# Optimization experiments

Measured on AMD Instinct MI355X. Metric: run time of the kernel, lower is better.

Reference implementation:

```python
import jax, jax.numpy as jnp
import numpy as np

NUM_HEADS = 16


def setup_inputs() -> dict:
    key = jax.random.key(0)
    ks = jax.random.split(key, 7)
    dim, hd = 1024, 64
    B, H, W = 64, 14, 14  # B = batch * num_windows, 14x14 window
    x = jax.random.normal(ks[0], (B, H, W, dim), dtype=jnp.float32)
    qkv_w = jax.random.normal(ks[1], (dim, 3 * dim), dtype=jnp.float32) * (dim ** -0.5)
    qkv_b = jnp.zeros((3 * dim,), dtype=jnp.float32)
    proj_w = jax.random.normal(ks[2], (dim, dim), dtype=jnp.float32) * (dim ** -0.5)
    proj_b = jnp.zeros((dim,), dtype=jnp.float32)
    rel_pos_h = jax.random.normal(ks[3], (2 * H - 1, hd), dtype=jnp.float32) * 0.02
    rel_pos_w = jax.random.normal(ks[4], (2 * W - 1, hd), dtype=jnp.float32) * 0.02
    return {"x": x, "qkv_w": qkv_w, "qkv_b": qkv_b, "proj_w": proj_w,
            "proj_b": proj_b, "rel_pos_h": rel_pos_h, "rel_pos_w": rel_pos_w}


def reference(x, qkv_w, qkv_b, proj_w, proj_b, rel_pos_h, rel_pos_w):
    B, H, W, dim = x.shape
    nH = NUM_HEADS
    hd = dim // nH
    scale = hd ** -0.5

    # qkv projection: [B, HW, 3*dim]
    qkv = x.reshape(B, H * W, dim) @ qkv_w + qkv_b
    # -> [3, nH, B, HW, hd] -> [3, nH*B, HW, hd]
    qkv = qkv.reshape(B, H * W, 3, nH, hd).transpose(2, 3, 0, 1, 4)
    qkv = qkv.reshape(3, nH * B, H * W, hd)
    q, k, v = qkv[0], qkv[1], qkv[2]

    # scaled QK^T: [nH*B, HW, HW]
    attn = jnp.einsum('bqc,bkc->bqk', q * scale, k)

    # decomposed relative position bias (q_size == k_size, no interpolation)
    Rh = rel_pos_h[jnp.arange(H)[:, None] - jnp.arange(H)[None, :] + (H - 1)]  # [H,H,hd]
    Rw = rel_pos_w[jnp.arange(W)[:, None] - jnp.arange(W)[None, :] + (W - 1)]  # [W,W,hd]
    r_q = q.reshape(nH * B, H, W, hd)
    rel_h = jnp.einsum('bhwc,hkc->bhwk', r_q, Rh)  # [nH*B,H,W,H]
    rel_w = jnp.einsum('bhwc,wkc->bhwk', r_q, Rw)  # [nH*B,H,W,W]
    attn = (attn.reshape(nH * B, H, W, H, W)
            + rel_h[:, :, :, :, None]
            + rel_w[:, :, :, None, :]).reshape(nH * B, H * W, H * W)

    attn = jax.nn.softmax(attn, axis=-1)
    out = attn @ v  # [nH*B, HW, hd]

    # merge heads: [nH,B,H,W,hd] -> [B,H,W,dim]
    out = out.reshape(nH, B, H, W, hd).transpose(1, 2, 3, 0, 4).reshape(B, H, W, dim)
    return out @ proj_w + proj_b
```

## Files before the change

### kernel.cpp

```cpp
#include <hip/hip_runtime.h>
#include <cstdint>
#include <cstddef>

typedef unsigned short u16;
typedef unsigned int u32;
typedef float f32x4 __attribute__((ext_vector_type(4)));
typedef short short8 __attribute__((ext_vector_type(8)));
typedef u32 u32x2 __attribute__((ext_vector_type(2)));

#define HW 196
#define DIM 1024
#define HD 64
#define SP 208
#define SPV 224
#define NBH 1024

__device__ __forceinline__ float bf2f(u16 x){
  union { u32 u; float f; } c; c.u = ((u32)x) << 16; return c.f;
}
__device__ __forceinline__ u16 f2bf(float f){
  union { float f; u32 u; } c; c.f = f;
  return (u16)((c.u + 0x7fffu + ((c.u >> 16) & 1u)) >> 16);
}
__device__ __forceinline__ u32 cvtpk_bf16(float lo, float hi){
  u32 r;
  asm("v_cvt_pk_bf16_f32 %0, %1, %2" : "=v"(r) : "v"(lo), "v"(hi));
  return r;
}
#define LGKM_FENCE() do { \
    asm volatile("s_waitcnt lgkmcnt(0)" ::: "memory"); \
    __builtin_amdgcn_sched_barrier(0); \
  } while (0)
#define DS_FENCE() do { \
    asm volatile("s_waitcnt lgkmcnt(0)" ::: "memory"); \
    __builtin_amdgcn_sched_barrier(0x7F); \
  } while (0)
#define WAITV4() asm volatile("s_waitcnt vmcnt(4)" ::: "memory")
#define BAR() __builtin_amdgcn_s_barrier()

typedef __attribute__((address_space(3))) void lds_void_t;
typedef __attribute__((address_space(1))) const void glb_void_t;
__device__ __forceinline__ void gload_lds16(const void* g, void* l){
  __builtin_amdgcn_global_load_lds((glb_void_t*)g, (lds_void_t*)l, 16, 0, 0);
}

__global__ __launch_bounds__(256) void k_xcvt(const float* __restrict__ x,
                                              u16* __restrict__ xb, int n8){
  int i = blockIdx.x * 256 + threadIdx.x;
  if (i < n8){
    const f32x4* p = (const f32x4*)(x + (size_t)i * 8);
    f32x4 v0 = p[0], v1 = p[1];
    short8 t;
    #pragma unroll
    for (int e = 0; e < 4; ++e){
      t[e]   = (short)f2bf(v0[e]);
      t[4+e] = (short)f2bf(v1[e]);
    }
    *(short8*)(xb + (size_t)i * 8) = t;
  }
}

__global__ __launch_bounds__(256) void k_rprep(const float* __restrict__ rph,
                                               const float* __restrict__ rpw,
                                               u16* __restrict__ rphb,
                                               u16* __restrict__ rpwb){
  int r = threadIdx.x >> 3, cc = (threadIdx.x & 7) * 8;
  #pragma unroll
  for (int t = 0; t < 2; ++t){
    const float* src = t ? rpw : rph;
    u16* dst = t ? rpwb : rphb;
    short8 v;
    #pragma unroll
    for (int e = 0; e < 8; ++e)
      v[e] = (r < 27) ? (short)f2bf(src[(size_t)r * 64 + cc + e]) : (short)0;
    *(short8*)(dst + (size_t)r * 64 + cc) = v;
  }
}

__global__ __launch_bounds__(256) void k_wT(const float* __restrict__ w,
                                            u16* __restrict__ wT, int K, int N){
  __shared__ float t[32][33];
  int n0 = blockIdx.x * 32, k0 = blockIdx.y * 32;
  int c = threadIdx.x & 31, rr = threadIdx.x >> 5;
  #pragma unroll
  for (int i = 0; i < 4; ++i){
    int r = rr + i*8;
    t[r][c] = w[(size_t)(k0 + r) * N + n0 + c];
  }
  __syncthreads();
  #pragma unroll
  for (int i = 0; i < 4; ++i){
    int r = rr + i*8;
    wT[(size_t)(n0 + r) * K + k0 + c] = f2bf(t[c][r]);
  }
}

template<int MODE, bool SW>
__global__ __launch_bounds__(512, 2) void k_g256(const u16* __restrict__ Ab,
    const u16* __restrict__ Bt, const float* __restrict__ bias,
    u16* __restrict__ qg, u16* __restrict__ kg, u16* __restrict__ vTg,
    float* __restrict__ outf, int K, int N, int ntm, int ntn, int cyoff)
{
  extern __shared__ __align__(16) u16 smem[];
  const int tid = threadIdx.x;
  const int lane = tid & 63, wv = tid >> 6;
  const int wr = wv >> 2, wc = wv & 3;
  const int l16 = lane & 15, lk = lane >> 4;

  const int nwg = ntm * ntn;
  int bid = blockIdx.x;
  int q8 = nwg >> 3, r8 = nwg & 7;
  int xcd = bid & 7, loc = bid >> 3;
  int wgid = (xcd < r8 ? xcd*(q8+1) : r8*(q8+1) + (xcd - r8)*q8) + loc;
  int gsz = 8 * ntn;
  int g = wgid / gsz, rem = wgid - g * gsz;
  int gm = ntm - g * 8; if (gm > 8) gm = 8;
  int ry = g * 8 + rem % gm;
  int cy = rem / gm;
  const size_t m0 = (size_t)ry * 256;
  const size_t n0 = (size_t)(cyoff + cy) * 256;
  const int nk = K >> 6;

  auto off = [&](int d, int ab, int ks){ return ((d*2 + ab)*2 + ks) * 8192; };

  auto stageH = [&](int d, int ab, int ks, int tile){
    const u16* src = ab ? Bt : Ab;
    size_t rb = ab ? n0 : m0;
    int c = (lane & 3) ^ ((lane >> 3) & 3);
    #pragma unroll
    for (int i = 0; i < 2; ++i){
      int rh = 32*wv + 16*i + (lane >> 2);
      gload_lds16(src + (rb + rh) * (size_t)K + tile*64 + ks*32 + c*8,
                  smem + off(d, ab, ks) + (32*wv + 16*i) * 32);
    }
  };
  auto ldA = [&](short8* a, int d, int ks, int h){
    #pragma unroll
    for (int m2 = 0; m2 < 4; ++m2){
      int r = wr*128 + h*64 + m2*16 + l16;
      a[m2] = *(const short8*)(smem + off(d,0,ks) + r*32 + ((lk ^ ((r>>1)&3)) << 3));
    }
  };
  auto ldB = [&](short8* b, int d, int ks){
    #pragma unroll
    for (int ni = 0; ni < 4; ++ni){
      int r = wc*64 + ni*16 + l16;
      b[ni] = *(const short8*)(smem + off(d,1,ks) + r*32 + ((lk ^ ((r>>1)&3)) << 3));
    }
  };

  f32x4 acc[8][4] = {};
  auto mm = [&](int h, short8* a, short8* b){
    __builtin_amdgcn_s_setprio(1);
    #pragma unroll
    for (int m2 = 0; m2 < 4; ++m2)
      #pragma unroll
      for (int ni = 0; ni < 4; ++ni){
        if constexpr (SW)
          acc[h*4+m2][ni] = __builtin_amdgcn_mfma_f32_16x16x32_bf16(b[ni], a[m2], acc[h*4+m2][ni], 0, 0, 0);
        else
          acc[h*4+m2][ni] = __builtin_amdgcn_mfma_f32_16x16x32_bf16(a[m2], b[ni], acc[h*4+m2][ni], 0, 0, 0);
      }
    __builtin_amdgcn_s_setprio(0);
  };

  stageH(0, 0, 0, 0); stageH(0, 1, 0, 0); stageH(0, 0, 1, 0); stageH(0, 1, 1, 0);
  WAITV4(); BAR();

  #pragma unroll 1
  for (int kt = 0; kt < nk; ++kt){
    const int d = kt & 1, dn = d ^ 1;
    const int tn = (kt + 1 < nk) ? kt + 1 : nk - 1;
    short8 a[4], b0[4], b1[4];
    ldA(a, d, 0, 0); ldB(b0, d, 0);
    stageH(dn, 0, 0, tn);
    BAR(); LGKM_FENCE();
    mm(0, a, b0);
    BAR();
    ldA(a, d, 0, 1);
    stageH(dn, 1, 0, tn);
    WAITV4();
    BAR(); LGKM_FENCE();
    mm(1, a, b0);
    BAR();
    ldA(a, d, 1, 0); ldB(b1, d, 1);
    stageH(dn, 0, 1, tn);
    BAR(); LGKM_FENCE();
    mm(0, a, b1);
    BAR();
    ldA(a, d, 1, 1);
    stageH(dn, 1, 1, tn);
    WAITV4();
    BAR(); LGKM_FENCE();
    mm(1, a, b1);
    BAR();
  }

  const int rowb = (int)m0 + wr*128;
  const int colb = (int)n0 + wc*64;
  if constexpr (MODE == 1){
    #pragma unroll
    for (int mi = 0; mi < 8; ++mi){
      int r = rowb + mi*16 + l16;
      float* orow = outf + (size_t)r * N;
      #pragma unroll
      for (int ni = 0; ni < 4; ++ni){
        int c0 = colb + ni*16 + lk*4;
        f32x4 bz = *(const f32x4*)(bias + c0);
        f32x4 v = acc[mi][ni] + bz;
        *(f32x4*)(orow + c0) = v;
      }
    }
  } else if constexpr (SW){
    const int t3 = colb >> 10;
    u16* dst0 = (t3 == 0) ? qg : kg;
    const float sc = (t3 == 0) ? 1.0f : 0.125f;
    #pragma unroll
    for (int mi = 0; mi < 8; ++mi){
      int r = rowb + mi*16 + l16;
      int b = r / 196, n = r - b * 196;
      #pragma unroll
      for (int ni = 0; ni < 4; ++ni){
        int rr2 = ((colb & 1023) + ni*16);
        int hh = rr2 >> 6, ccb = (rr2 & 63) + lk*4;
        const float* bz = bias + colb + ni*16 + lk*4;
        u32 w0 = cvtpk_bf16((acc[mi][ni][0] + bz[0])*sc, (acc[mi][ni][1] + bz[1])*sc);
        u32 w1 = cvtpk_bf16((acc[mi][ni][2] + bz[2])*sc, (acc[mi][ni][3] + bz[3])*sc);
        u32* dst = (u32*)(dst0 + ((size_t)(hh*64 + b) * SP + n) * HD + ccb);
        dst[0] = w0; dst[1] = w1;
      }
    }
  } else {
    #pragma unroll
    for (int mi = 0; mi < 8; ++mi){
      int r4 = rowb + mi*16 + lk*4;
      int b = r4 / 196, n4 = r4 - b * 196;
      #pragma unroll
      for (int ni = 0; ni < 4; ++ni){
        int rr2 = ((colb & 1023) + ni*16);
        int hh = rr2 >> 6, cc = (rr2 & 63) + l16;
        float bz = bias[colb + ni*16 + l16];
        u32 w0 = cvtpk_bf16(acc[mi][ni][0] + bz, acc[mi][ni][1] + bz);
        u32 w1 = cvtpk_bf16(acc[mi][ni][2] + bz, acc[mi][ni][3] + bz);
        u32* dst = (u32*)(vTg + ((size_t)(hh*64 + b) * HD + cc) * SPV + n4);
        dst[0] = w0; dst[1] = w1;
      }
    }
  }
}

__global__ __launch_bounds__(256) void k_attn(
    const u16* __restrict__ qg, const u16* __restrict__ kg, const u16* __restrict__ vTg,
    const u16* __restrict__ rphb, const u16* __restrict__ rpwb,
    u16* __restrict__ ao)
{
  __shared__ __align__(16) char smem[4 * 7424];
  const int tid = threadIdx.x, lane = tid & 63, wvi = tid >> 6;
  const int l16 = lane & 15, lk = lane >> 4;
  char*  wbase = smem + wvi * 7424;
  float* relT  = (float*)wbase;
  u32*   Pp    = (u32*)wbase;

  int b = blockIdx.x;
  int sb = (b & 7) * 416 + (b >> 3);
  int j  = sb * 4 + wvi;
  int bh = j / 13;
  int mt = j - bh * 13;
  const int hh = bh >> 6, bb = bh & 63;
  const u16* qb = qg  + (size_t)bh * SP * HD;
  const u16* kb = kg  + (size_t)bh * SP * HD;
  const u16* vb = vTg + (size_t)bh * HD * SPV;

  const short8 a0 = *(const short8*)(qb + (size_t)(mt*16 + l16) * HD + lk*8);
  const short8 a1 = *(const short8*)(qb + (size_t)(mt*16 + l16) * HD + 32 + lk*8);

  {
    f32x4 z = {0.f,0.f,0.f,0.f};
    f32x4 racc[2][2] = {{z,z},{z,z}};
    #pragma unroll
    for (int dt = 0; dt < 2; ++dt){
      short8 h0 = *(const short8*)(rphb + (size_t)(dt*16 + l16) * 64 + lk*8);
      short8 h1 = *(const short8*)(rphb + (size_t)(dt*16 + l16) * 64 + 32 + lk*8);
      short8 w0 = *(const short8*)(rpwb + (size_t)(dt*16 + l16) * 64 + lk*8);
      short8 w1 = *(const short8*)(rpwb + (size_t)(dt*16 + l16) * 64 + 32 + lk*8);
      racc[0][dt] = __builtin_amdgcn_mfma_f32_16x16x32_bf16(h0, a0, racc[0][dt], 0, 0, 0);
      racc[0][dt] = __builtin_amdgcn_mfma_f32_16x16x32_bf16(h1, a1, racc[0][dt], 0, 0, 0);
      racc[1][dt] = __builtin_amdgcn_mfma_f32_16x16x32_bf16(w0, a0, racc[1][dt], 0, 0, 0);
      racc[1][dt] = __builtin_amdgcn_mfma_f32_16x16x32_bf16(w1, a1, racc[1][dt], 0, 0, 0);
    }
    #pragma unroll
    for (int t = 0; t < 2; ++t)
      #pragma unroll
      for (int dt = 0; dt < 2; ++dt)
        *(f32x4*)(relT + l16*68 + t*32 + dt*16 + lk*4) = racc[t][dt];
  }
  DS_FENCE();

  int qr = mt*16 + l16;
  int qrc = qr > HW-1 ? HW-1 : qr;
  int qh = qrc / 14, qw = qrc - 14*qh;
  const float* rrow = relT + l16*68;
  const int dh0 = qh + 13, dw0 = 32 + qw + 13;
  const int lk4 = lk*4;

  f32x4 sacc[13];
  #pragma unroll
  for (int nt = 0; nt < 13; ++nt){
    #pragma unroll
    for (int i = 0; i < 4; ++i){
      int k = nt*16 + lk4 + i;
      int kh = (k * 4682) >> 16;
      if (nt == 12 && kh > 13) kh = 13;
      int kw = k - kh*14;
      float bias = rrow[dh0 - kh] + rrow[dw0 - kw];
      sacc[nt][i] = (nt == 12 && lk != 0) ? -1e30f : bias;
    }
  }

  #pragma unroll
  for (int nt = 0; nt < 13; ++nt){
    int row = nt*16 + l16;
    short8 b0 = *(const short8*)(kb + (size_t)row * HD + lk*8);
    short8 b1 = *(const short8*)(kb + (size_t)row * HD + 32 + lk*8);
    sacc[nt] = __builtin_amdgcn_mfma_f32_16x16x32_bf16(b0, a0, sacc[nt], 0, 0, 0);
    sacc[nt] = __builtin_amdgcn_mfma_f32_16x16x32_bf16(b1, a1, sacc[nt], 0, 0, 0);
  }

  float m;
  {
    float t0[13];
    #pragma unroll
    for (int nt = 0; nt < 13; ++nt)
      t0[nt] = fmaxf(fmaxf(sacc[nt][0], sacc[nt][1]), fmaxf(sacc[nt][2], sacc[nt][3]));
    float a01 = fmaxf(t0[0], t0[1]),  a23 = fmaxf(t0[2], t0[3]);
    float a45 = fmaxf(t0[4], t0[5]),  a67 = fmaxf(t0[6], t0[7]);
    float a89 = fmaxf(t0[8], t0[9]),  aab = fmaxf(t0[10], t0[11]);
    m = fmaxf(fmaxf(fmaxf(a01, a23), fmaxf(a45, a67)), fmaxf(fmaxf(a89, aab), t0[12]));
  }
  m = fmaxf(m, __shfl_xor(m, 16, 64));
  m = fmaxf(m, __shfl_xor(m, 32, 64));
  float sum;
  {
    float s4[13];
    #pragma unroll
    for (int nt = 0; nt < 13; ++nt){
      #pragma unroll
      for (int i = 0; i < 4; ++i)
        sacc[nt][i] = __expf(sacc[nt][i] - m);
      s4[nt] = (sacc[nt][0] + sacc[nt][1]) + (sacc[nt][2] + sacc[nt][3]);
    }
    float b01 = s4[0]+s4[1], b23 = s4[2]+s4[3], b45 = s4[4]+s4[5];
    float b67 = s4[6]+s4[7], b89 = s4[8]+s4[9], bab = s4[10]+s4[11];
    sum = ((b01+b23) + (b45+b67)) + ((b89+bab) + s4[12]);
  }
  sum += __shfl_xor(sum, 16, 64);
  sum += __shfl_xor(sum, 32, 64);
  float inv = 1.0f / sum;

  DS_FENCE();
  u32* prow = Pp + l16*116;
  #pragma unroll
  for (int nt = 0; nt < 13; ++nt){
    u32x2 wpk;
    wpk[0] = cvtpk_bf16(sacc[nt][0], sacc[nt][1]);
    wpk[1] = cvtpk_bf16(sacc[nt][2], sacc[nt][3]);
    *(u32x2*)(prow + nt*8 + lk*2) = wpk;
  }
  { u32x2 zz = {0u, 0u}; *(u32x2*)(prow + 104 + lk*2) = zz; }
  DS_FENCE();

  f32x4 z = {0.f,0.f,0.f,0.f};
  f32x4 oacc[4] = {z,z,z,z};
  #pragma unroll
  for (int kt = 0; kt < 7; ++kt){
    short8 pa = *(const short8*)(prow + kt*16 + lk4);
    #pragma unroll
    for (int dt = 0; dt < 4; ++dt){
      short8 bv = *(const short8*)(vb + (size_t)(dt*16 + l16) * SPV + kt*32 + lk*8);
      oacc[dt] = __builtin_amdgcn_mfma_f32_16x16x32_bf16(bv, pa, oacc[dt], 0, 0, 0);
    }
  }
  int qrow = mt*16 + l16;
  if (qrow < HW){
    u16* orow = ao + ((size_t)bb * HW + qrow) * DIM + hh * HD;
    #pragma unroll
    for (int dt = 0; dt < 4; ++dt){
      u32 lo = cvtpk_bf16(oacc[dt][0]*inv, oacc[dt][1]*inv);
      u32 hi = cvtpk_bf16(oacc[dt][2]*inv, oacc[dt][3]*inv);
      u32* dst = (u32*)(orow + dt*16 + lk4);
      dst[0] = lo; dst[1] = hi;
    }
  }
}

extern "C" void kernel_launch(void* const* d_in, const int* in_sizes, int n_in,
                              void* d_out, int out_size, void* d_ws, size_t ws_size,
                              hipStream_t stream)
{
  const float* x      = (const float*)d_in[0];
  const float* qkv_w  = (const float*)d_in[1];
  const float* qkv_b  = (const float*)d_in[2];
  const float* proj_w = (const float*)d_in[3];
  const float* proj_b = (const float*)d_in[4];
  const float* rph    = (const float*)d_in[5];
  const float* rpw    = (const float*)d_in[6];
  float* out = (float*)d_out;
  char* ws = (char*)d_ws;

  size_t off = 0;
  auto alloc = [&](size_t b){ size_t r = off; off += (b + 255) & ~(size_t)255; return r; };
  u16* wqkvT = (u16*)(ws + alloc((size_t)3072*1024*2));
  u16* wprojT= (u16*)(ws + alloc((size_t)1024*1024*2));
  u16* qg    = (u16*)(ws + alloc((size_t)NBH*SP*HD*2));
  u16* kg    = (u16*)(ws + alloc((size_t)NBH*SP*HD*2));
  u16* vTg   = (u16*)(ws + alloc((size_t)NBH*HD*SPV*2));
  u16* rphb  = (u16*)(ws + alloc((size_t)32*64*2));
  u16* rpwb  = (u16*)(ws + alloc((size_t)32*64*2));
  u16* xb    = (u16*)(ws + alloc((size_t)12544*1024*2));
  u16* ao    = xb;

  hipFuncSetAttribute((const void*)k_g256<0,true>,  hipFuncAttributeMaxDynamicSharedMemorySize, 131072);
  hipFuncSetAttribute((const void*)k_g256<0,false>, hipFuncAttributeMaxDynamicSharedMemorySize, 131072);
  hipFuncSetAttribute((const void*)k_g256<1,true>,  hipFuncAttributeMaxDynamicSharedMemorySize, 131072);

  hipMemsetAsync(vTg, 0, (size_t)NBH*HD*SPV*2, stream);

  k_xcvt<<<(12544*1024/8 + 255)/256, 256, 0, stream>>>(x, xb, 12544*1024/8);
  k_wT<<<dim3(96, 32), 256, 0, stream>>>(qkv_w, wqkvT, 1024, 3072);
  k_wT<<<dim3(32, 32), 256, 0, stream>>>(proj_w, wprojT, 1024, 1024);
  k_rprep<<<1, 256, 0, stream>>>(rph, rpw, rphb, rpwb);

  k_g256<0,true><<<49*8, 512, 131072, stream>>>(xb, wqkvT, qkv_b, qg, kg, nullptr, nullptr,
                                                1024, 3072, 49, 8, 0);
  k_g256<0,false><<<49*4, 512, 131072, stream>>>(xb, wqkvT, qkv_b, nullptr, nullptr, vTg, nullptr,
                                                 1024, 3072, 49, 4, 8);
  k_attn<<<3328, 256, 0, stream>>>(qg, kg, vTg, rphb, rpwb, ao);
  k_g256<1,true><<<49*4, 512, 131072, stream>>>(ao, wprojT, proj_b, nullptr, nullptr, nullptr, out,
                                                1024, 1024, 49, 4, 0);
}
```

Measured before the change: 257.1 us.

## Merge QKV GEMMs into one launch and stage K/V in LDS per head

The separate Q/K and V projection launches are merged into one GEMM launch covering all 3072 columns. The V tile now uses the same MFMA operand order as Q/K and writes the transposed V layout with scalar bf16 stores. The attention kernel now runs one 832-thread block (13 waves) per batch-head and copies K and V into padded LDS once, so the 13 query tiles no longer each read K and V from global memory. In exchange the kernel needs about 156KB of dynamic shared memory, which limits it to one block per CU, and the V epilogue stores are narrower and strided.

```diff
diff --git a/kernel.cpp b/kernel.cpp
--- a/kernel.cpp
+++ b/kernel.cpp
@@ -95,11 +95,11 @@
   }
 }
 
-template<int MODE, bool SW>
+template<int MODE>
 __global__ __launch_bounds__(512, 2) void k_g256(const u16* __restrict__ Ab,
     const u16* __restrict__ Bt, const float* __restrict__ bias,
     u16* __restrict__ qg, u16* __restrict__ kg, u16* __restrict__ vTg,
-    float* __restrict__ outf, int K, int N, int ntm, int ntn, int cyoff)
+    float* __restrict__ outf, int K, int N, int ntm, int ntn)
 {
   extern __shared__ __align__(16) u16 smem[];
   const int tid = threadIdx.x;
@@ -118,7 +118,7 @@
   int ry = g * 8 + rem % gm;
   int cy = rem / gm;
   const size_t m0 = (size_t)ry * 256;
-  const size_t n0 = (size_t)(cyoff + cy) * 256;
+  const size_t n0 = (size_t)cy * 256;
   const int nk = K >> 6;
 
   auto off = [&](int d, int ab, int ks){ return ((d*2 + ab)*2 + ks) * 8192; };
@@ -155,12 +155,8 @@
     #pragma unroll
     for (int m2 = 0; m2 < 4; ++m2)
       #pragma unroll
-      for (int ni = 0; ni < 4; ++ni){
-        if constexpr (SW)
-          acc[h*4+m2][ni] = __builtin_amdgcn_mfma_f32_16x16x32_bf16(b[ni], a[m2], acc[h*4+m2][ni], 0, 0, 0);
-        else
-          acc[h*4+m2][ni] = __builtin_amdgcn_mfma_f32_16x16x32_bf16(a[m2], b[ni], acc[h*4+m2][ni], 0, 0, 0);
-      }
+      for (int ni = 0; ni < 4; ++ni)
+        acc[h*4+m2][ni] = __builtin_amdgcn_mfma_f32_16x16x32_bf16(b[ni], a[m2], acc[h*4+m2][ni], 0, 0, 0);
     __builtin_amdgcn_s_setprio(0);
   };
 
@@ -211,66 +207,83 @@
         *(f32x4*)(orow + c0) = v;
       }
     }
-  } else if constexpr (SW){
+  } else {
     const int t3 = colb >> 10;
-    u16* dst0 = (t3 == 0) ? qg : kg;
-    const float sc = (t3 == 0) ? 1.0f : 0.125f;
-    #pragma unroll
-    for (int mi = 0; mi < 8; ++mi){
-      int r = rowb + mi*16 + l16;
-      int b = r / 196, n = r - b * 196;
-      #pragma unroll
-      for (int ni = 0; ni < 4; ++ni){
-        int rr2 = ((colb & 1023) + ni*16);
-        int hh = rr2 >> 6, ccb = (rr2 & 63) + lk*4;
-        const float* bz = bias + colb + ni*16 + lk*4;
-        u32 w0 = cvtpk_bf16((acc[mi][ni][0] + bz[0])*sc, (acc[mi][ni][1] + bz[1])*sc);
-        u32 w1 = cvtpk_bf16((acc[mi][ni][2] + bz[2])*sc, (acc[mi][ni][3] + bz[3])*sc);
-        u32* dst = (u32*)(dst0 + ((size_t)(hh*64 + b) * SP + n) * HD + ccb);
-        dst[0] = w0; dst[1] = w1;
+    if (t3 < 2){
+      u16* dst0 = (t3 == 0) ? qg : kg;
+      const float sc = (t3 == 0) ? 1.0f : 0.125f;
+      #pragma unroll
+      for (int mi = 0; mi < 8; ++mi){
+        int r = rowb + mi*16 + l16;
+        int b = r / 196, n = r - b * 196;
+        #pragma unroll
+        for (int ni = 0; ni < 4; ++ni){
+          int rr2 = ((colb & 1023) + ni*16);
+          int hh = rr2 >> 6, ccb = (rr2 & 63) + lk*4;
+          const float* bz = bias + colb + ni*16 + lk*4;
+          u32 w0 = cvtpk_bf16((acc[mi][ni][0] + bz[0])*sc, (acc[mi][ni][1] + bz[1])*sc);
+          u32 w1 = cvtpk_bf16((acc[mi][ni][2] + bz[2])*sc, (acc[mi][ni][3] + bz[3])*sc);
+          u32* dst = (u32*)(dst0 + ((size_t)(hh*64 + b) * SP + n) * HD + ccb);
+          dst[0] = w0; dst[1] = w1;
+        }
       }
-    }
-  } else {
-    #pragma unroll
-    for (int mi = 0; mi < 8; ++mi){
-      int r4 = rowb + mi*16 + lk*4;
-      int b = r4 / 196, n4 = r4 - b * 196;
-      #pragma unroll
-      for (int ni = 0; ni < 4; ++ni){
-        int rr2 = ((colb & 1023) + ni*16);
-        int hh = rr2 >> 6, cc = (rr2 & 63) + l16;
-        float bz = bias[colb + ni*16 + l16];
-        u32 w0 = cvtpk_bf16(acc[mi][ni][0] + bz, acc[mi][ni][1] + bz);
-        u32 w1 = cvtpk_bf16(acc[mi][ni][2] + bz, acc[mi][ni][3] + bz);
-        u32* dst = (u32*)(vTg + ((size_t)(hh*64 + b) * HD + cc) * SPV + n4);
-        dst[0] = w0; dst[1] = w1;
+    } else {
+      #pragma unroll
+      for (int mi = 0; mi < 8; ++mi){
+        int r = rowb + mi*16 + l16;
+        int b = r / 196, n = r - b * 196;
+        #pragma unroll
+        for (int ni = 0; ni < 4; ++ni){
+          int col0 = colb + ni*16 + lk*4;
+          f32x4 bz = *(const f32x4*)(bias + col0);
+          int rem2 = col0 & 1023;
+          int hh = rem2 >> 6, cc0 = rem2 & 63;
+          u16* base = vTg + ((size_t)(hh*64 + b) * HD + cc0) * SPV + n;
+          #pragma unroll
+          for (int i = 0; i < 4; ++i)
+            base[(size_t)i * SPV] = f2bf(acc[mi][ni][i] + bz[i]);
+        }
       }
     }
   }
 }
 
-__global__ __launch_bounds__(256) void k_attn(
+#define KSTR 144
+#define VSTR 464
+#define PWB  7424
+__global__ __launch_bounds__(832, 1) void k_attn(
     const u16* __restrict__ qg, const u16* __restrict__ kg, const u16* __restrict__ vTg,
     const u16* __restrict__ rphb, const u16* __restrict__ rpwb,
     u16* __restrict__ ao)
 {
-  __shared__ __align__(16) char smem[4 * 7424];
+  extern __shared__ __align__(16) char asmem[];
+  char* Klds = asmem;
+  char* Vlds = asmem + 29952;
   const int tid = threadIdx.x, lane = tid & 63, wvi = tid >> 6;
   const int l16 = lane & 15, lk = lane >> 4;
-  char*  wbase = smem + wvi * 7424;
+  char*  wbase = asmem + 59648 + wvi * PWB;
   float* relT  = (float*)wbase;
   u32*   Pp    = (u32*)wbase;
 
-  int b = blockIdx.x;
-  int sb = (b & 7) * 416 + (b >> 3);
-  int j  = sb * 4 + wvi;
-  int bh = j / 13;
-  int mt = j - bh * 13;
+  const int bh = blockIdx.x;
   const int hh = bh >> 6, bb = bh & 63;
   const u16* qb = qg  + (size_t)bh * SP * HD;
   const u16* kb = kg  + (size_t)bh * SP * HD;
   const u16* vb = vTg + (size_t)bh * HD * SPV;
 
+  for (int c = tid; c < 1664; c += 832){
+    int row = c >> 3, colb = (c & 7) << 4;
+    short8 d = *(const short8*)((const char*)kb + row*128 + colb);
+    *(short8*)(Klds + row*KSTR + colb) = d;
+  }
+  for (int c = tid; c < 1792; c += 832){
+    int row = c / 28, colb = (c - row*28) << 4;
+    short8 d = *(const short8*)((const char*)vb + row*448 + colb);
+    *(short8*)(Vlds + row*VSTR + colb) = d;
+  }
+  __syncthreads();
+
+  const int mt = wvi;
   const short8 a0 = *(const short8*)(qb + (size_t)(mt*16 + l16) * HD + lk*8);
   const short8 a1 = *(const short8*)(qb + (size_t)(mt*16 + l16) * HD + 32 + lk*8);
 
@@ -320,8 +333,8 @@
   #pragma unroll
   for (int nt = 0; nt < 13; ++nt){
     int row = nt*16 + l16;
-    short8 b0 = *(const short8*)(kb + (size_t)row * HD + lk*8);
-    short8 b1 = *(const short8*)(kb + (size_t)row * HD + 32 + lk*8);
+    short8 b0 = *(const short8*)(Klds + row*KSTR + lk*16);
+    short8 b1 = *(const short8*)(Klds + row*KSTR + 64 + lk*16);
     sacc[nt] = __builtin_amdgcn_mfma_f32_16x16x32_bf16(b0, a0, sacc[nt], 0, 0, 0);
     sacc[nt] = __builtin_amdgcn_mfma_f32_16x16x32_bf16(b1, a1, sacc[nt], 0, 0, 0);
   }
@@ -376,7 +389,7 @@
     short8 pa = *(const short8*)(prow + kt*16 + lk4);
     #pragma unroll
     for (int dt = 0; dt < 4; ++dt){
-      short8 bv = *(const short8*)(vb + (size_t)(dt*16 + l16) * SPV + kt*32 + lk*8);
+      short8 bv = *(const short8*)(Vlds + (dt*16 + l16)*VSTR + kt*64 + lk*16);
       oacc[dt] = __builtin_amdgcn_mfma_f32_16x16x32_bf16(bv, pa, oacc[dt], 0, 0, 0);
     }
   }
@@ -419,9 +432,9 @@
   u16* xb    = (u16*)(ws + alloc((size_t)12544*1024*2));
   u16* ao    = xb;
 
-  hipFuncSetAttribute((const void*)k_g256<0,true>,  hipFuncAttributeMaxDynamicSharedMemorySize, 131072);
-  hipFuncSetAttribute((const void*)k_g256<0,false>, hipFuncAttributeMaxDynamicSharedMemorySize, 131072);
-  hipFuncSetAttribute((const void*)k_g256<1,true>,  hipFuncAttributeMaxDynamicSharedMemorySize, 131072);
+  hipFuncSetAttribute((const void*)k_g256<0>, hipFuncAttributeMaxDynamicSharedMemorySize, 131072);
+  hipFuncSetAttribute((const void*)k_g256<1>, hipFuncAttributeMaxDynamicSharedMemorySize, 131072);
+  hipFuncSetAttribute((const void*)k_attn,    hipFuncAttributeMaxDynamicSharedMemorySize, 156160);
 
   hipMemsetAsync(vTg, 0, (size_t)NBH*HD*SPV*2, stream);
 
@@ -430,11 +443,9 @@
   k_wT<<<dim3(32, 32), 256, 0, stream>>>(proj_w, wprojT, 1024, 1024);
   k_rprep<<<1, 256, 0, stream>>>(rph, rpw, rphb, rpwb);
 
-  k_g256<0,true><<<49*8, 512, 131072, stream>>>(xb, wqkvT, qkv_b, qg, kg, nullptr, nullptr,
-                                                1024, 3072, 49, 8, 0);
-  k_g256<0,false><<<49*4, 512, 131072, stream>>>(xb, wqkvT, qkv_b, nullptr, nullptr, vTg, nullptr,
-                                                 1024, 3072, 49, 4, 8);
-  k_attn<<<3328, 256, 0, stream>>>(qg, kg, vTg, rphb, rpwb, ao);
-  k_g256<1,true><<<49*4, 512, 131072, stream>>>(ao, wprojT, proj_b, nullptr, nullptr, nullptr, out,
-                                                1024, 1024, 49, 4, 0);
-}
+  k_g256<0><<<49*12, 512, 131072, stream>>>(xb, wqkvT, qkv_b, qg, kg, vTg, nullptr,
+                                            1024, 3072, 49, 12);
+  k_attn<<<1024, 832, 156160, stream>>>(qg, kg, vTg, rphb, rpwb, ao);
+  k_g256<1><<<49*4, 512, 131072, stream>>>(ao, wprojT, proj_b, nullptr, nullptr, nullptr, out,
+                                           1024, 1024, 49, 4);
+}
```

After: 228.0 us. 11.3% less time.
